# Performance work log

Measured on AMD Instinct MI355X. Metric: run time of the kernel, lower is better.

Reference implementation:

```python
import jax, jax.numpy as jnp
import numpy as np

N_NODES = 100000
N_EDGES = 1200000
N_GRAPHS = 1000
NUM_SHAPES, NUM_COLORS, NUM_CLASSES = 16, 8, 10


def setup_inputs() -> dict:
    key = jax.random.key(0)
    ks = jax.random.split(key, 12)
    x = jax.random.randint(ks[0], (N_NODES, 2), 0, 8, dtype=jnp.int32)
    edge_index = jax.random.randint(ks[1], (2, N_EDGES), 0, N_NODES, dtype=jnp.int32)
    batch = jnp.sort(jax.random.randint(ks[2], (N_NODES,), 0, N_GRAPHS, dtype=jnp.int32))
    s = 0.05
    params = {
        "shape_emb": jax.random.normal(ks[3], (NUM_SHAPES, 8), jnp.float32) * s,
        "color_emb": jax.random.normal(ks[4], (NUM_COLORS, 8), jnp.float32) * s,
        "W_pre": jax.random.normal(ks[5], (32, 16), jnp.float32) * s,
        "b_pre": jnp.zeros((32,), jnp.float32),
        "W_rel1": jax.random.normal(ks[6], (64, 32), jnp.float32) * s,
        "b_rel1": jnp.zeros((64,), jnp.float32),
        "W_root1": jax.random.normal(ks[7], (64, 32), jnp.float32) * s,
        "W_rel2": jax.random.normal(ks[8], (64, 64), jnp.float32) * s,
        "b_rel2": jnp.zeros((64,), jnp.float32),
        "W_root2": jax.random.normal(ks[9], (64, 64), jnp.float32) * s,
        "W_cls": jax.random.normal(ks[10], (NUM_CLASSES, 64), jnp.float32) * s,
        "b_cls": jnp.zeros((NUM_CLASSES,), jnp.float32),
    }
    return dict(x=x, edge_index=edge_index, batch=batch, num_graphs=N_GRAPHS, **params)


def _graph_conv(h, src, dst, W_rel, b_rel, W_root, n_nodes):
    # PyG GraphConv: out = lin_rel(sum_{j in N(i)} x_j) + lin_root(x_i)
    agg = jax.ops.segment_sum(h[src], dst, num_segments=n_nodes)  # [N, d_in]
    return agg @ W_rel.T + b_rel + h @ W_root.T


def reference(x, edge_index, batch, num_graphs,
              shape_emb, color_emb, W_pre, b_pre,
              W_rel1, b_rel1, W_root1, W_rel2, b_rel2, W_root2,
              W_cls, b_cls):
    n_nodes = x.shape[0]
    src, dst = edge_index[0], edge_index[1]
    h = jnp.concatenate([shape_emb[x[:, 0]], color_emb[x[:, 1]]], axis=1)  # [N, 16]
    h = jax.nn.relu(h @ W_pre.T + b_pre)                                    # [N, 32]
    h = jax.nn.relu(_graph_conv(h, src, dst, W_rel1, b_rel1, W_root1, n_nodes))  # [N, 64]
    h = jax.nn.relu(_graph_conv(h, src, dst, W_rel2, b_rel2, W_root2, n_nodes))  # [N, 64]
    # global mean pool over graphs
    sums = jax.ops.segment_sum(h, batch, num_segments=num_graphs)           # [G, 64]
    counts = jax.ops.segment_sum(jnp.ones((n_nodes,), h.dtype), batch, num_segments=num_graphs)
    pooled = sums / jnp.maximum(counts, 1.0)[:, None]
    return pooled @ W_cls.T + b_cls                                         # [G, num_classes]
```

## Files before the change

kernel.cpp:

```cpp
#include <hip/hip_runtime.h>
#include <hip/hip_bf16.h>


#define NGRAPHS 1000
#define SCAN_CHUNK 4096

typedef _Float16 f16x8 __attribute__((ext_vector_type(8)));
typedef float f32x4 __attribute__((ext_vector_type(4)));

__global__ __launch_bounds__(256) void k_hist(const int* __restrict__ dst,
                                              int* __restrict__ hist,
                                              int* __restrict__ rank, int nE)
{
    int e = blockIdx.x * 256 + threadIdx.x;
    if (e < nE) rank[e] = atomicAdd(&hist[dst[e]], 1);
}

__global__ __launch_bounds__(256) void k_scan_part(const int* __restrict__ hist,
                                                   int* __restrict__ bsum, int n)
{
    __shared__ int s[256];
    int t = threadIdx.x;
    int beg = blockIdx.x * SCAN_CHUNK + t * 16;
    int sum = 0;
#pragma unroll
    for (int q = 0; q < 16; ++q) {
        int i = beg + q;
        if (i < n) sum += hist[i];
    }
    s[t] = sum;
    __syncthreads();
    for (int off = 128; off > 0; off >>= 1) {
        if (t < off) s[t] += s[t + off];
        __syncthreads();
    }
    if (t == 0) bsum[blockIdx.x] = s[0];
}

__global__ __launch_bounds__(64) void k_scan_mid(const int* __restrict__ bsum,
                                                 int* __restrict__ boffs,
                                                 int* __restrict__ row_ptr,
                                                 int B, int n)
{
    if (threadIdx.x == 0) {
        int run = 0;
        for (int b = 0; b < B; ++b) {
            boffs[b] = run;
            run += bsum[b];
        }
        row_ptr[n] = run;
    }
}

__global__ __launch_bounds__(256) void k_scan_apply(const int* __restrict__ hist,
                                                    const int* __restrict__ boffs,
                                                    int* __restrict__ row_ptr, int n)
{
    __shared__ int s[256];
    int t = threadIdx.x;
    int beg = blockIdx.x * SCAN_CHUNK + t * 16;
    int v[16];
    int sum = 0;
#pragma unroll
    for (int q = 0; q < 16; ++q) {
        int i = beg + q;
        v[q] = (i < n) ? hist[i] : 0;
        sum += v[q];
    }
    s[t] = sum;
    __syncthreads();
    for (int off = 1; off < 256; off <<= 1) {
        int x = (t >= off) ? s[t - off] : 0;
        __syncthreads();
        s[t] += x;
        __syncthreads();
    }
    int base = boffs[blockIdx.x] + ((t == 0) ? 0 : s[t - 1]);
#pragma unroll
    for (int q = 0; q < 16; ++q) {
        int i = beg + q;
        if (i < n) {
            row_ptr[i] = base;
            base += v[q];
        }
    }
}

__global__ __launch_bounds__(256) void k_scatteridx(
    const int* __restrict__ src, const int* __restrict__ dst,
    const int* __restrict__ row_ptr, const int* __restrict__ rank,
    int* __restrict__ sorted_src, int nE)
{
    int e = blockIdx.x * 256 + threadIdx.x;
    if (e >= nE) return;
    int d = dst[e];
    sorted_src[row_ptr[d] + rank[e]] = src[e];
}

__global__ __launch_bounds__(256) void k_pre(
    const int* __restrict__ x,
    const float* __restrict__ shape_emb, const float* __restrict__ color_emb,
    const float* __restrict__ W_pre, const float* __restrict__ b_pre,
    _Float16* __restrict__ h1, int n)
{
    __shared__ float sW[32 * 16];
    __shared__ float sB[32];
    __shared__ float sSE[16 * 8];
    __shared__ float sCE[8 * 8];
    int t = threadIdx.x;
    for (int i = t; i < 32 * 16; i += 256) sW[i] = W_pre[i];
    if (t < 32) sB[t] = b_pre[t];
    for (int i = t; i < 16 * 8; i += 256) sSE[i] = shape_emb[i];
    if (t < 64) sCE[t] = color_emb[t];
    __syncthreads();

    int i = blockIdx.x * 256 + t;
    if (i >= n) return;
    int s = x[2 * i];
    int c = x[2 * i + 1];
    float in[16];
#pragma unroll
    for (int k = 0; k < 8; ++k) in[k] = sSE[s * 8 + k];
#pragma unroll
    for (int k = 0; k < 8; ++k) in[8 + k] = sCE[c * 8 + k];

    float acc[32];
#pragma unroll
    for (int j = 0; j < 32; ++j) acc[j] = sB[j];
#pragma unroll
    for (int k = 0; k < 16; ++k) {
        float v = in[k];
#pragma unroll
        for (int j = 0; j < 32; ++j) acc[j] += sW[j * 16 + k] * v;
    }
#pragma unroll
    for (int g = 0; g < 4; ++g) {
        f16x8 o;
#pragma unroll
        for (int q = 0; q < 8; ++q) o[q] = (_Float16)fmaxf(acc[g * 8 + q], 0.f);
        *(f16x8*)(h1 + (size_t)i * 32 + g * 8) = o;
    }
}

template <int WIDTH, int PARTS>
__global__ __launch_bounds__(256) void k_agg(
    const int* __restrict__ row_ptr, const int* __restrict__ sorted_src,
    const _Float16* __restrict__ h, _Float16* __restrict__ agg, int n)
{
    int tid = blockIdx.x * 256 + threadIdx.x;
    int i = tid / PARTS;
    int p = tid % PARTS;
    if (i >= n) return;
    float a[8] = {0, 0, 0, 0, 0, 0, 0, 0};
    float b[8] = {0, 0, 0, 0, 0, 0, 0, 0};
    int e0 = row_ptr[i], e1 = row_ptr[i + 1];
    const _Float16* hp = h + p * 8;
    int e = e0;
    for (; e + 4 <= e1; e += 4) {
        int s0 = sorted_src[e];
        int s1 = sorted_src[e + 1];
        int s2 = sorted_src[e + 2];
        int s3 = sorted_src[e + 3];
        f16x8 r0 = *(const f16x8*)(hp + (size_t)s0 * WIDTH);
        f16x8 r1 = *(const f16x8*)(hp + (size_t)s1 * WIDTH);
        f16x8 r2 = *(const f16x8*)(hp + (size_t)s2 * WIDTH);
        f16x8 r3 = *(const f16x8*)(hp + (size_t)s3 * WIDTH);
#pragma unroll
        for (int q = 0; q < 8; ++q) {
            a[q] += (float)r0[q] + (float)r2[q];
            b[q] += (float)r1[q] + (float)r3[q];
        }
    }
    for (; e < e1; ++e) {
        int s0 = sorted_src[e];
        f16x8 r0 = *(const f16x8*)(hp + (size_t)s0 * WIDTH);
#pragma unroll
        for (int q = 0; q < 8; ++q) a[q] += (float)r0[q];
    }
    f16x8 o;
#pragma unroll
    for (int q = 0; q < 8; ++q) o[q] = (_Float16)(a[q] + b[q]);
    *(f16x8*)(agg + (size_t)i * WIDTH + p * 8) = o;
}

template <int WIN>
__global__ __launch_bounds__(256) void k_conv_mfma(
    const _Float16* __restrict__ agg, const _Float16* __restrict__ h,
    const float* __restrict__ W_rel, const float* __restrict__ b_rel,
    const float* __restrict__ W_root, _Float16* __restrict__ out, int n)
{
    constexpr int NK = (2 * WIN) / 32;
    int t = threadIdx.x;
    int lane = t & 63;
    int w = t >> 6;
    int col = lane & 15;
    int krow = lane >> 4;

    f16x8 B[NK][4];
#pragma unroll
    for (int ks = 0; ks < NK; ++ks) {
#pragma unroll
        for (int ct = 0; ct < 4; ++ct) {
            int j = ct * 16 + col;
            int kb = ks * 32 + krow * 8;
            const float* srcw = (ks < NK / 2)
                ? (W_rel + (size_t)j * WIN + kb)
                : (W_root + (size_t)j * WIN + (kb - WIN));
            float4 w0 = *(const float4*)(srcw);
            float4 w1 = *(const float4*)(srcw + 4);
            f16x8 bb;
            bb[0] = (_Float16)w0.x; bb[1] = (_Float16)w0.y;
            bb[2] = (_Float16)w0.z; bb[3] = (_Float16)w0.w;
            bb[4] = (_Float16)w1.x; bb[5] = (_Float16)w1.y;
            bb[6] = (_Float16)w1.z; bb[7] = (_Float16)w1.w;
            B[ks][ct] = bb;
        }
        __builtin_amdgcn_sched_barrier(0);
    }

    float bias[4];
#pragma unroll
    for (int ct = 0; ct < 4; ++ct) bias[ct] = b_rel[ct * 16 + col];

    int nodebase = blockIdx.x * 128 + w * 32;

    f32x4 acc[2][4];
#pragma unroll
    for (int nt = 0; nt < 2; ++nt)
#pragma unroll
        for (int ct = 0; ct < 4; ++ct) acc[nt][ct] = (f32x4){0.f, 0.f, 0.f, 0.f};

#pragma unroll
    for (int ks = 0; ks < NK; ++ks) {
        const _Float16* base = (ks < NK / 2) ? agg : h;
        int koff = ((ks < NK / 2) ? ks : ks - NK / 2) * 32 + krow * 8;
#pragma unroll
        for (int nt = 0; nt < 2; ++nt) {
            int i = nodebase + nt * 16 + col;
            i = min(i, n - 1);
            f16x8 a = *(const f16x8*)(base + (size_t)i * WIN + koff);
#pragma unroll
            for (int ct = 0; ct < 4; ++ct)
                acc[nt][ct] = __builtin_amdgcn_mfma_f32_16x16x32_f16(
                    a, B[ks][ct], acc[nt][ct], 0, 0, 0);
        }
    }

#pragma unroll
    for (int nt = 0; nt < 2; ++nt) {
#pragma unroll
        for (int r = 0; r < 4; ++r) {
            int node = nodebase + nt * 16 + krow * 4 + r;
            if (node < n) {
#pragma unroll
                for (int ct = 0; ct < 4; ++ct) {
                    float v = acc[nt][ct][r] + bias[ct];
                    out[(size_t)node * 64 + ct * 16 + col] = (_Float16)fmaxf(v, 0.f);
                }
            }
        }
    }
}

__global__ __launch_bounds__(256) void k_pool_cls(
    const _Float16* __restrict__ h3, const int* __restrict__ batch,
    const float* __restrict__ W_cls, const float* __restrict__ b_cls,
    float* __restrict__ out, int n)
{
    __shared__ float part[4][64];
    __shared__ float pool[64];
    __shared__ int range[2];
    int g = blockIdx.x;
    int t = threadIdx.x;

    if (t < 2) {
        int key = g + t;
        int lo = 0, hi = n;
        while (lo < hi) {
            int mid = (lo + hi) >> 1;
            if (batch[mid] < key) lo = mid + 1; else hi = mid;
        }
        range[t] = lo;
    }
    __syncthreads();
    int start = range[0], end = range[1];

    int j = t & 63;
    int sub = t >> 6;
    float local = 0.f;
    for (int i = start + sub; i < end; i += 4)
        local += (float)h3[(size_t)i * 64 + j];
    part[sub][j] = local;
    __syncthreads();

    if (t < 64) {
        float cnt = (float)(end - start);
        float inv = 1.0f / fmaxf(cnt, 1.0f);
        pool[t] = (part[0][t] + part[1][t] + part[2][t] + part[3][t]) * inv;
    }
    __syncthreads();

    if (t < 10) {
        float acc = b_cls[t];
#pragma unroll
        for (int k = 0; k < 64; ++k) acc += W_cls[t * 64 + k] * pool[k];
        out[(size_t)g * 10 + t] = acc;
    }
}

extern "C" void kernel_launch(void* const* d_in, const int* in_sizes, int n_in,
                              void* d_out, int out_size, void* d_ws, size_t ws_size,
                              hipStream_t stream)
{
    const int* x        = (const int*)d_in[0];
    const int* ei       = (const int*)d_in[1];
    const int* batch    = (const int*)d_in[2];
    const float* shape_emb = (const float*)d_in[4];
    const float* color_emb = (const float*)d_in[5];
    const float* W_pre   = (const float*)d_in[6];
    const float* b_pre   = (const float*)d_in[7];
    const float* W_rel1  = (const float*)d_in[8];
    const float* b_rel1  = (const float*)d_in[9];
    const float* W_root1 = (const float*)d_in[10];
    const float* W_rel2  = (const float*)d_in[11];
    const float* b_rel2  = (const float*)d_in[12];
    const float* W_root2 = (const float*)d_in[13];
    const float* W_cls   = (const float*)d_in[14];
    const float* b_cls   = (const float*)d_in[15];

    const int n  = in_sizes[0] / 2;
    const int nE = in_sizes[1] / 2;
    const int G  = NGRAPHS;
    const int* src = ei;
    const int* dst = ei + nE;

    _Float16* us = (_Float16*)d_ws;
    _Float16* h1B   = us;
    _Float16* agg1B = h1B + (size_t)n * 32;
    _Float16* h2B   = us + (size_t)n * 64;
    _Float16* agg2B = us + (size_t)n * 128;
    _Float16* h3B   = us;
    int* ints       = (int*)(us + (size_t)n * 192);
    int* row_ptr    = ints;
    int* hist       = ints + (n + 1);
    int* rank       = ints + (n + 1) + n;
    int* sorted_src = rank + nE;
    int* bsum       = sorted_src + nE;
    int* boffs      = bsum + 64;

    const int EB = (nE + 255) / 256;
    const int NB = (n + 255) / 256;
    const int CB = (n + 127) / 128;
    const int SB = (n + SCAN_CHUNK - 1) / SCAN_CHUNK;

    hipMemsetAsync(hist, 0, (size_t)n * sizeof(int), stream);
    k_hist<<<EB, 256, 0, stream>>>(dst, hist, rank, nE);
    k_scan_part<<<SB, 256, 0, stream>>>(hist, bsum, n);
    k_scan_mid<<<1, 64, 0, stream>>>(bsum, boffs, row_ptr, SB, n);
    k_scan_apply<<<SB, 256, 0, stream>>>(hist, boffs, row_ptr, n);
    k_scatteridx<<<EB, 256, 0, stream>>>(src, dst, row_ptr, rank, sorted_src, nE);

    k_pre<<<NB, 256, 0, stream>>>(x, shape_emb, color_emb, W_pre, b_pre, h1B, n);
    k_agg<32, 4><<<((size_t)n * 4 + 255) / 256, 256, 0, stream>>>(row_ptr, sorted_src, h1B, agg1B, n);
    k_conv_mfma<32><<<CB, 256, 0, stream>>>(agg1B, h1B, W_rel1, b_rel1, W_root1, h2B, n);
    k_agg<64, 8><<<((size_t)n * 8 + 255) / 256, 256, 0, stream>>>(row_ptr, sorted_src, h2B, agg2B, n);
    k_conv_mfma<64><<<CB, 256, 0, stream>>>(agg2B, h2B, W_rel2, b_rel2, W_root2, h3B, n);
    k_pool_cls<<<G, 256, 0, stream>>>(h3B, batch, W_cls, b_cls, (float*)d_out, n);
}
```

Measured before the change: 273.7 us.

## Aggregate first layer from 128-entry embedding table and spread histogram atomics across copies

Node features after the pre-layer depend only on the (shape, color) pair, so the first aggregation looks up a 128-row fp16 table held in shared memory, indexed by a 7-bit code packed into the high bits of each sorted edge entry, instead of gathering h1 rows from global memory. The degree histogram is split into 8 copies selected by block index to reduce atomic contention, followed by a combine pass that computes per-copy offsets. The packing assumes node ids fit in 17 bits, shape index below 16 and color below 8. It adds an 8x larger histogram memset and an extra combine kernel.

```diff
diff --git a/kernel.cpp b/kernel.cpp
--- a/kernel.cpp
+++ b/kernel.cpp
@@ -4,16 +4,34 @@
 
 #define NGRAPHS 1000
 #define SCAN_CHUNK 4096
+#define SRCMASK 0x1FFFF
 
 typedef _Float16 f16x8 __attribute__((ext_vector_type(8)));
 typedef float f32x4 __attribute__((ext_vector_type(4)));
 
-__global__ __launch_bounds__(256) void k_hist(const int* __restrict__ dst,
-                                              int* __restrict__ hist,
-                                              int* __restrict__ rank, int nE)
+__global__ __launch_bounds__(256) void k_hist8(const int* __restrict__ dst,
+                                               int* __restrict__ hist8,
+                                               int* __restrict__ rank, int n, int nE)
 {
     int e = blockIdx.x * 256 + threadIdx.x;
-    if (e < nE) rank[e] = atomicAdd(&hist[dst[e]], 1);
+    if (e >= nE) return;
+    int copy = blockIdx.x & 7;
+    rank[e] = atomicAdd(&hist8[(size_t)copy * n + dst[e]], 1);
+}
+
+__global__ __launch_bounds__(256) void k_combine(int* __restrict__ hist8,
+                                                 int* __restrict__ total, int n)
+{
+    int i = blockIdx.x * 256 + threadIdx.x;
+    if (i >= n) return;
+    int s = 0;
+#pragma unroll
+    for (int c = 0; c < 8; ++c) {
+        int v = hist8[(size_t)c * n + i];
+        hist8[(size_t)c * n + i] = s;
+        s += v;
+    }
+    total[i] = s;
 }
 
 __global__ __launch_bounds__(256) void k_scan_part(const int* __restrict__ hist,
@@ -88,20 +106,24 @@
 
 __global__ __launch_bounds__(256) void k_scatteridx(
     const int* __restrict__ src, const int* __restrict__ dst,
-    const int* __restrict__ row_ptr, const int* __restrict__ rank,
-    int* __restrict__ sorted_src, int nE)
+    const int* __restrict__ row_ptr, const int* __restrict__ hist8,
+    const int* __restrict__ rank, const int* __restrict__ code,
+    int* __restrict__ sorted, int n, int nE)
 {
     int e = blockIdx.x * 256 + threadIdx.x;
     if (e >= nE) return;
+    int copy = blockIdx.x & 7;
     int d = dst[e];
-    sorted_src[row_ptr[d] + rank[e]] = src[e];
+    int s = src[e];
+    int pos = row_ptr[d] + hist8[(size_t)copy * n + d] + rank[e];
+    sorted[pos] = (code[s] << 17) | s;
 }
 
 __global__ __launch_bounds__(256) void k_pre(
     const int* __restrict__ x,
     const float* __restrict__ shape_emb, const float* __restrict__ color_emb,
     const float* __restrict__ W_pre, const float* __restrict__ b_pre,
-    _Float16* __restrict__ h1, int n)
+    _Float16* __restrict__ h1, int* __restrict__ code, int n)
 {
     __shared__ float sW[32 * 16];
     __shared__ float sB[32];
@@ -118,6 +140,7 @@
     if (i >= n) return;
     int s = x[2 * i];
     int c = x[2 * i + 1];
+    code[i] = (s << 3) | (c & 7);
     float in[16];
 #pragma unroll
     for (int k = 0; k < 8; ++k) in[k] = sSE[s * 8 + k];
@@ -142,9 +165,78 @@
     }
 }
 
+__global__ __launch_bounds__(128) void k_table(
+    const float* __restrict__ shape_emb, const float* __restrict__ color_emb,
+    const float* __restrict__ W_pre, const float* __restrict__ b_pre,
+    _Float16* __restrict__ table)
+{
+    int c = threadIdx.x;
+    int si = c >> 3, ci = c & 7;
+    float in[16];
+#pragma unroll
+    for (int k = 0; k < 8; ++k) in[k] = shape_emb[si * 8 + k];
+#pragma unroll
+    for (int k = 0; k < 8; ++k) in[8 + k] = color_emb[ci * 8 + k];
+    float acc[32];
+#pragma unroll
+    for (int j = 0; j < 32; ++j) acc[j] = b_pre[j];
+#pragma unroll
+    for (int k = 0; k < 16; ++k) {
+        float v = in[k];
+#pragma unroll
+        for (int j = 0; j < 32; ++j) acc[j] += W_pre[j * 16 + k] * v;
+    }
+#pragma unroll
+    for (int g = 0; g < 4; ++g) {
+        f16x8 o;
+#pragma unroll
+        for (int q = 0; q < 8; ++q) o[q] = (_Float16)fmaxf(acc[g * 8 + q], 0.f);
+        *(f16x8*)(table + (size_t)c * 32 + g * 8) = o;
+    }
+}
+
+__global__ __launch_bounds__(256) void k_agg1_tab(
+    const int* __restrict__ row_ptr, const int* __restrict__ sorted,
+    const _Float16* __restrict__ table, _Float16* __restrict__ agg, int n)
+{
+    __shared__ _Float16 tab[128 * 32];
+    int t = threadIdx.x;
+    for (int i = t * 8; i < 128 * 32; i += 256 * 8)
+        *(f16x8*)(tab + i) = *(const f16x8*)(table + i);
+    __syncthreads();
+
+    int tid = blockIdx.x * 256 + t;
+    int i = tid >> 2;
+    int p = tid & 3;
+    if (i >= n) return;
+    float a[8] = {0, 0, 0, 0, 0, 0, 0, 0};
+    float b[8] = {0, 0, 0, 0, 0, 0, 0, 0};
+    int e0 = row_ptr[i], e1 = row_ptr[i + 1];
+    const _Float16* tp = tab + p * 8;
+    int e = e0;
+    for (; e + 2 <= e1; e += 2) {
+        int c0 = sorted[e] >> 17;
+        int c1 = sorted[e + 1] >> 17;
+        f16x8 r0 = *(const f16x8*)(tp + c0 * 32);
+        f16x8 r1 = *(const f16x8*)(tp + c1 * 32);
+#pragma unroll
+        for (int q = 0; q < 8; ++q) { a[q] += (float)r0[q]; b[q] += (float)r1[q]; }
+    }
+    if (e < e1) {
+        int c0 = sorted[e] >> 17;
+        f16x8 r0 = *(const f16x8*)(tp + c0 * 32);
+#pragma unroll
+        for (int q = 0; q < 8; ++q) a[q] += (float)r0[q];
+    }
+    f16x8 o;
+#pragma unroll
+    for (int q = 0; q < 8; ++q) o[q] = (_Float16)(a[q] + b[q]);
+    *(f16x8*)(agg + (size_t)i * 32 + p * 8) = o;
+}
+
 template <int WIDTH, int PARTS>
 __global__ __launch_bounds__(256) void k_agg(
-    const int* __restrict__ row_ptr, const int* __restrict__ sorted_src,
+    const int* __restrict__ row_ptr, const int* __restrict__ sorted,
     const _Float16* __restrict__ h, _Float16* __restrict__ agg, int n)
 {
     int tid = blockIdx.x * 256 + threadIdx.x;
@@ -157,10 +249,10 @@
     const _Float16* hp = h + p * 8;
     int e = e0;
     for (; e + 4 <= e1; e += 4) {
-        int s0 = sorted_src[e];
-        int s1 = sorted_src[e + 1];
-        int s2 = sorted_src[e + 2];
-        int s3 = sorted_src[e + 3];
+        int s0 = sorted[e] & SRCMASK;
+        int s1 = sorted[e + 1] & SRCMASK;
+        int s2 = sorted[e + 2] & SRCMASK;
+        int s3 = sorted[e + 3] & SRCMASK;
         f16x8 r0 = *(const f16x8*)(hp + (size_t)s0 * WIDTH);
         f16x8 r1 = *(const f16x8*)(hp + (size_t)s1 * WIDTH);
         f16x8 r2 = *(const f16x8*)(hp + (size_t)s2 * WIDTH);
@@ -172,7 +264,7 @@
         }
     }
     for (; e < e1; ++e) {
-        int s0 = sorted_src[e];
+        int s0 = sorted[e] & SRCMASK;
         f16x8 r0 = *(const f16x8*)(hp + (size_t)s0 * WIDTH);
 #pragma unroll
         for (int q = 0; q < 8; ++q) a[q] += (float)r0[q];
@@ -336,34 +428,39 @@
 
     _Float16* us = (_Float16*)d_ws;
     _Float16* h1B   = us;
-    _Float16* agg1B = h1B + (size_t)n * 32;
+    _Float16* agg1B = us + (size_t)n * 32;
     _Float16* h2B   = us + (size_t)n * 64;
     _Float16* agg2B = us + (size_t)n * 128;
     _Float16* h3B   = us;
-    int* ints       = (int*)(us + (size_t)n * 192);
-    int* row_ptr    = ints;
-    int* hist       = ints + (n + 1);
-    int* rank       = ints + (n + 1) + n;
-    int* sorted_src = rank + nE;
-    int* bsum       = sorted_src + nE;
-    int* boffs      = bsum + 64;
+    _Float16* tabB  = us + (size_t)n * 192;
+    int* ints    = (int*)(tabB + 128 * 32);
+    int* code    = ints;
+    int* row_ptr = code + n;
+    int* hist8   = row_ptr + (n + 1);
+    int* total   = hist8 + (size_t)8 * n;
+    int* rank    = total + n;
+    int* sorted  = rank + nE;
+    int* bsum    = sorted + nE;
+    int* boffs   = bsum + 64;
 
     const int EB = (nE + 255) / 256;
     const int NB = (n + 255) / 256;
     const int CB = (n + 127) / 128;
     const int SB = (n + SCAN_CHUNK - 1) / SCAN_CHUNK;
 
-    hipMemsetAsync(hist, 0, (size_t)n * sizeof(int), stream);
-    k_hist<<<EB, 256, 0, stream>>>(dst, hist, rank, nE);
-    k_scan_part<<<SB, 256, 0, stream>>>(hist, bsum, n);
+    hipMemsetAsync(hist8, 0, (size_t)8 * n * sizeof(int), stream);
+    k_pre<<<NB, 256, 0, stream>>>(x, shape_emb, color_emb, W_pre, b_pre, h1B, code, n);
+    k_table<<<1, 128, 0, stream>>>(shape_emb, color_emb, W_pre, b_pre, tabB);
+    k_hist8<<<EB, 256, 0, stream>>>(dst, hist8, rank, n, nE);
+    k_combine<<<NB, 256, 0, stream>>>(hist8, total, n);
+    k_scan_part<<<SB, 256, 0, stream>>>(total, bsum, n);
     k_scan_mid<<<1, 64, 0, stream>>>(bsum, boffs, row_ptr, SB, n);
-    k_scan_apply<<<SB, 256, 0, stream>>>(hist, boffs, row_ptr, n);
-    k_scatteridx<<<EB, 256, 0, stream>>>(src, dst, row_ptr, rank, sorted_src, nE);
-
-    k_pre<<<NB, 256, 0, stream>>>(x, shape_emb, color_emb, W_pre, b_pre, h1B, n);
-    k_agg<32, 4><<<((size_t)n * 4 + 255) / 256, 256, 0, stream>>>(row_ptr, sorted_src, h1B, agg1B, n);
+    k_scan_apply<<<SB, 256, 0, stream>>>(total, boffs, row_ptr, n);
+    k_scatteridx<<<EB, 256, 0, stream>>>(src, dst, row_ptr, hist8, rank, code, sorted, n, nE);
+
+    k_agg1_tab<<<((size_t)n * 4 + 255) / 256, 256, 0, stream>>>(row_ptr, sorted, tabB, agg1B, n);
     k_conv_mfma<32><<<CB, 256, 0, stream>>>(agg1B, h1B, W_rel1, b_rel1, W_root1, h2B, n);
-    k_agg<64, 8><<<((size_t)n * 8 + 255) / 256, 256, 0, stream>>>(row_ptr, sorted_src, h2B, agg2B, n);
+    k_agg<64, 8><<<((size_t)n * 8 + 255) / 256, 256, 0, stream>>>(row_ptr, sorted, h2B, agg2B, n);
     k_conv_mfma<64><<<CB, 256, 0, stream>>>(agg2B, h2B, W_rel2, b_rel2, W_root2, h3B, n);
     k_pool_cls<<<G, 256, 0, stream>>>(h3B, batch, W_cls, b_cls, (float*)d_out, n);
 }
```

Result: slower. 291.7 us (+6.6%).
